# Performance work log

Measured on AMD Instinct MI355X. Metric: run time of the kernel, lower is better.

## Reference

```python
import jax, jax.numpy as jnp
import numpy as np

N = 8192
F_IN = 256
F_OUT = 64
ALPHA = 0.2  # LeakyReLU negative slope
NEG_INF = -9e15


def setup_inputs() -> dict:
    key = jax.random.key(0)
    k1, k2, k3, k4 = jax.random.split(key, 4)
    h = jax.random.normal(k1, (N, F_IN), dtype=jnp.float32)
    adj = jax.random.randint(k2, (N, N), 0, 2, dtype=jnp.int32)
    W = jax.random.normal(k3, (F_IN, F_OUT), dtype=jnp.float32) * 0.1
    a = jax.random.normal(k4, (2 * F_OUT, 1), dtype=jnp.float32) * 0.1
    return {"h": h, "adj": adj, "W": W, "a": a}


def reference(h, adj, W, a):
    # Wh: [N, F_out]
    Wh = h @ W
    # e_ij = LeakyReLU(a1 . Wh_i + a2 . Wh_j); same math as the O(N^2*2F)
    # concat in the original, computed via two [N] gathers + broadcast add.
    f_src = Wh @ a[:F_OUT, 0]   # [N] contribution of node i (row)
    f_dst = Wh @ a[F_OUT:, 0]   # [N] contribution of node j (col)
    e = f_src[:, None] + f_dst[None, :]          # [N, N]
    e = jnp.where(e > 0, e, ALPHA * e)           # LeakyReLU
    # masked softmax over neighbors (dim=1)
    e = jnp.where(adj > 0, e, NEG_INF)
    attention = jax.nn.softmax(e, axis=1)        # [N, N]
    h_prime = attention @ Wh                     # [N, F_out]
    # concat=True -> ELU
    return jax.nn.elu(h_prime)
```

## Files before the change

kernel.cpp:

```cpp
#include <hip/hip_runtime.h>
#include <math.h>

#define N 8192
#define FIN 256
#define FOUT 64
#define ALPHA 0.2f
#define LOG2E 1.442695040888963f

#define JT 256
#define NTILE (N / JT)
#define ROWPITCH 512
#define OFF_B 0
#define OFF_A (64 * ROWPITCH)
#define SMEM_BYTES (OFF_A + 16 * ROWPITCH)

typedef float f32x4 __attribute__((ext_vector_type(4)));
typedef _Float16 f16x8 __attribute__((ext_vector_type(8)));

__device__ __forceinline__ unsigned pack_f16(float a, float b) {
    union { _Float16 h; unsigned short u; } ca, cb;
    ca.h = (_Float16)a; cb.h = (_Float16)b;
    return (unsigned)ca.u | ((unsigned)cb.u << 16);
}
__device__ __forceinline__ float wcalc(int av, float fsr, float g) {
    float e = fsr + g;
    float le = e > 0.f ? e : ALPHA * e;
    float r = __builtin_exp2f(fmaf(le, LOG2E, -4.0f));
    return av != 0 ? r : 0.f;
}

__global__ __launch_bounds__(256) void gat_prep(
    const float* __restrict__ h, const float* __restrict__ W,
    const float* __restrict__ a,
    float* __restrict__ fsrc, float* __restrict__ fdst,
    unsigned short* __restrict__ WhT)
{
    __shared__ float sWh[16][FOUT + 1];
    const int t = threadIdx.x;
    const int f = t & 63;
    const int wq = t >> 6;
    const int row0 = blockIdx.x * 16;
    const int rbase = row0 + wq * 4;

    float acc[4] = {0.f, 0.f, 0.f, 0.f};
    for (int k0 = 0; k0 < FIN; k0 += 4) {
        const float w0 = W[(k0 + 0) * FOUT + f];
        const float w1 = W[(k0 + 1) * FOUT + f];
        const float w2 = W[(k0 + 2) * FOUT + f];
        const float w3 = W[(k0 + 3) * FOUT + f];
#pragma unroll
        for (int rr = 0; rr < 4; ++rr) {
            const float4 hv = *reinterpret_cast<const float4*>(
                &h[(size_t)(rbase + rr) * FIN + k0]);
            acc[rr] = fmaf(hv.x, w0, acc[rr]);
            acc[rr] = fmaf(hv.y, w1, acc[rr]);
            acc[rr] = fmaf(hv.z, w2, acc[rr]);
            acc[rr] = fmaf(hv.w, w3, acc[rr]);
        }
    }
    const float as = a[f], ad = a[FOUT + f];
#pragma unroll
    for (int rr = 0; rr < 4; ++rr) {
        sWh[wq * 4 + rr][f] = acc[rr];
        float fs = acc[rr] * as, fd = acc[rr] * ad;
#pragma unroll
        for (int off = 1; off < 64; off <<= 1) {
            fs += __shfl_xor(fs, off, 64);
            fd += __shfl_xor(fd, off, 64);
        }
        if (f == 0) { fsrc[rbase + rr] = fs; fdst[rbase + rr] = fd; }
    }
    __syncthreads();
    const int ff = t >> 2;
    const int r4 = (t & 3) * 4;
    uint2 v;
    v.x = pack_f16(sWh[r4 + 0][ff], sWh[r4 + 1][ff]);
    v.y = pack_f16(sWh[r4 + 2][ff], sWh[r4 + 3][ff]);
    *reinterpret_cast<uint2*>(&WhT[(size_t)ff * N + row0 + r4]) = v;
}

struct Regs { int4 a0, a1; float4 g0, g1; int4 b0, b1, b2, b3; };

__global__ __launch_bounds__(512, 4) void gat_main(
    const int* __restrict__ adj,
    const unsigned short* __restrict__ WhT,
    const float* __restrict__ fsrc, const float* __restrict__ fdst,
    float* __restrict__ out)
{
    __shared__ __align__(16) char smem[SMEM_BYTES];
    __shared__ float zbuf[16];

    const int t = threadIdx.x;
    const int l = t & 63;
    const int w = t >> 6;
    const int row0 = blockIdx.x * 16;

    const int srow = t >> 5;
    const int sc8 = (t & 31) * 8;
    const int bf = t >> 3;
    const int bg = t & 7;
    const float fsr = fsrc[row0 + srow];
    const size_t adjrow = (size_t)(row0 + srow) * N;
    const size_t bfrow = (size_t)bf * N;

    const int aswz = (srow & 7) << 4;
    const int bswz = (bf & 7) << 4;
    char* aw = smem + OFF_A + srow * ROWPITCH + (((t & 31) * 16) ^ aswz);
    char* bw0 = smem + OFF_B + bf * ROWPITCH + (((bg + 0) * 16) ^ bswz);
    char* bw1 = smem + OFF_B + bf * ROWPITCH + (((bg + 8) * 16) ^ bswz);
    char* bw2 = smem + OFF_B + bf * ROWPITCH + (((bg + 16) * 16) ^ bswz);
    char* bw3 = smem + OFF_B + bf * ROWPITCH + (((bg + 24) * 16) ^ bswz);

    const int ft = w & 3;
    const int p = w >> 2;
    const int r16 = l & 15;
    const int kg8 = (l >> 4) << 3;
    const int fswz = (r16 & 7) << 4;
    const char* ar = smem + OFF_A + r16 * ROWPITCH;
    const char* br = smem + OFF_B + (ft * 16 + r16) * ROWPITCH;

    f32x4 acc = {0.f, 0.f, 0.f, 0.f};
    float zacc = 0.f;
    Regs RA, RB;

#define LOADG(tile, S)                                                         \
    {                                                                          \
        const int j0_ = (tile) * JT;                                           \
        S.a0 = *reinterpret_cast<const int4*>(&adj[adjrow + j0_ + sc8]);       \
        S.a1 = *reinterpret_cast<const int4*>(&adj[adjrow + j0_ + sc8 + 4]);   \
        S.g0 = *reinterpret_cast<const float4*>(&fdst[j0_ + sc8]);             \
        S.g1 = *reinterpret_cast<const float4*>(&fdst[j0_ + sc8 + 4]);         \
        S.b0 = *reinterpret_cast<const int4*>(&WhT[bfrow + j0_ + (bg+0)*8]);   \
        S.b1 = *reinterpret_cast<const int4*>(&WhT[bfrow + j0_ + (bg+8)*8]);   \
        S.b2 = *reinterpret_cast<const int4*>(&WhT[bfrow + j0_ + (bg+16)*8]);  \
        S.b3 = *reinterpret_cast<const int4*>(&WhT[bfrow + j0_ + (bg+24)*8]);  \
    }

#define STAGE(S)                                                               \
    {                                                                          \
        *reinterpret_cast<int4*>(bw0) = S.b0;                                  \
        *reinterpret_cast<int4*>(bw1) = S.b1;                                  \
        *reinterpret_cast<int4*>(bw2) = S.b2;                                  \
        *reinterpret_cast<int4*>(bw3) = S.b3;                                  \
        const float w0 = wcalc(S.a0.x, fsr, S.g0.x);                           \
        const float w1 = wcalc(S.a0.y, fsr, S.g0.y);                           \
        const float w2 = wcalc(S.a0.z, fsr, S.g0.z);                           \
        const float w3 = wcalc(S.a0.w, fsr, S.g0.w);                           \
        const float w4 = wcalc(S.a1.x, fsr, S.g1.x);                           \
        const float w5 = wcalc(S.a1.y, fsr, S.g1.y);                           \
        const float w6 = wcalc(S.a1.z, fsr, S.g1.z);                           \
        const float w7 = wcalc(S.a1.w, fsr, S.g1.w);                           \
        zacc += (w0 + w1) + (w2 + w3) + ((w4 + w5) + (w6 + w7));               \
        uint4 pk;                                                              \
        pk.x = pack_f16(w0, w1); pk.y = pack_f16(w2, w3);                      \
        pk.z = pack_f16(w4, w5); pk.w = pack_f16(w6, w7);                      \
        *reinterpret_cast<uint4*>(aw) = pk;                                    \
    }

#define MFMA_PHASE                                                             \
    {                                                                          \
        __builtin_amdgcn_s_setprio(1);                                         \
        _Pragma("unroll")                                                      \
        for (int ks = 0; ks < 4; ++ks) {                                       \
            const int cb = (p * 128 + ks * 32 + kg8) * 2;                      \
            const f16x8 af = *reinterpret_cast<const f16x8*>(ar + (cb ^ fswz));\
            const f16x8 bfv = *reinterpret_cast<const f16x8*>(br + (cb ^ fswz));\
            acc = __builtin_amdgcn_mfma_f32_16x16x32_f16(af, bfv, acc, 0, 0, 0);\
        }                                                                      \
        __builtin_amdgcn_s_setprio(0);                                         \
    }

    LOADG(0, RA);
    LOADG(1, RB);
    for (int tt = 0; tt < NTILE; tt += 2) {
        STAGE(RA);
        if (tt + 2 < NTILE) LOADG(tt + 2, RA);
        __syncthreads();
        MFMA_PHASE;
        __syncthreads();
        STAGE(RB);
        if (tt + 3 < NTILE) LOADG(tt + 3, RB);
        __syncthreads();
        MFMA_PHASE;
        __syncthreads();
    }
#undef LOADG
#undef STAGE
#undef MFMA_PHASE

    {
        float z = zacc;
#pragma unroll
        for (int off = 1; off < 32; off <<= 1) z += __shfl_xor(z, off, 64);
        if ((l & 31) == 0) zbuf[srow] = z;
    }

    *reinterpret_cast<f32x4*>(smem + w * 1024 + l * 16) = acc;
    __syncthreads();
#pragma unroll
    for (int e0 = 0; e0 < 2; ++e0) {
        const int e = t + e0 * 512;
        const int rr = e >> 6, f2 = e & 63;
        const int ft2 = f2 >> 4, n = f2 & 15;
        const int ln = n | ((rr >> 2) << 4);
        const int rg = rr & 3;
        const float s =
            *reinterpret_cast<const float*>(smem + ft2 * 1024 + ln * 16 + rg * 4) +
            *reinterpret_cast<const float*>(smem + (ft2 + 4) * 1024 + ln * 16 + rg * 4);
        const float hp = s / zbuf[rr];
        out[(size_t)(row0 + rr) * FOUT + f2] = hp > 0.f ? hp : expm1f(hp);
    }
}

extern "C" void kernel_launch(void* const* d_in, const int* in_sizes, int n_in,
                              void* d_out, int out_size, void* d_ws, size_t ws_size,
                              hipStream_t stream) {
    const float* h   = (const float*)d_in[0];
    const int*   adj = (const int*)d_in[1];
    const float* W   = (const float*)d_in[2];
    const float* a   = (const float*)d_in[3];
    float* out = (float*)d_out;

    float* ws = (float*)d_ws;
    float* fsrc = ws;
    float* fdst = fsrc + N;
    unsigned short* WhT = (unsigned short*)(fdst + N);

    gat_prep<<<dim3(N / 16), dim3(256), 0, stream>>>(h, W, a, fsrc, fdst, WhT);
    gat_main<<<dim3(N / 16), dim3(512), 0, stream>>>(adj, WhT, fsrc, fdst, out);
}
```

Measured before the change: 97.20 us.

## Double-buffer LDS tiles and use one lightweight barrier per tile

```diff
diff --git a/kernel.cpp b/kernel.cpp
--- a/kernel.cpp
+++ b/kernel.cpp
@@ -12,7 +12,8 @@
 #define ROWPITCH 512
 #define OFF_B 0
 #define OFF_A (64 * ROWPITCH)
-#define SMEM_BYTES (OFF_A + 16 * ROWPITCH)
+#define BUFB (OFF_A + 16 * ROWPITCH)
+#define SMEM_BYTES (2 * BUFB)
 
 typedef float f32x4 __attribute__((ext_vector_type(4)));
 typedef _Float16 f16x8 __attribute__((ext_vector_type(8)));
@@ -88,7 +89,6 @@
     float* __restrict__ out)
 {
     __shared__ __align__(16) char smem[SMEM_BYTES];
-    __shared__ float zbuf[16];
 
     const int t = threadIdx.x;
     const int l = t & 63;
@@ -105,23 +105,29 @@
 
     const int aswz = (srow & 7) << 4;
     const int bswz = (bf & 7) << 4;
-    char* aw = smem + OFF_A + srow * ROWPITCH + (((t & 31) * 16) ^ aswz);
-    char* bw0 = smem + OFF_B + bf * ROWPITCH + (((bg + 0) * 16) ^ bswz);
-    char* bw1 = smem + OFF_B + bf * ROWPITCH + (((bg + 8) * 16) ^ bswz);
-    char* bw2 = smem + OFF_B + bf * ROWPITCH + (((bg + 16) * 16) ^ bswz);
-    char* bw3 = smem + OFF_B + bf * ROWPITCH + (((bg + 24) * 16) ^ bswz);
+    const int awo  = OFF_A + srow * ROWPITCH + (((t & 31) * 16) ^ aswz);
+    const int bwo0 = OFF_B + bf * ROWPITCH + (((bg + 0) * 16) ^ bswz);
+    const int bwo1 = OFF_B + bf * ROWPITCH + (((bg + 8) * 16) ^ bswz);
+    const int bwo2 = OFF_B + bf * ROWPITCH + (((bg + 16) * 16) ^ bswz);
+    const int bwo3 = OFF_B + bf * ROWPITCH + (((bg + 24) * 16) ^ bswz);
 
     const int ft = w & 3;
     const int p = w >> 2;
     const int r16 = l & 15;
     const int kg8 = (l >> 4) << 3;
     const int fswz = (r16 & 7) << 4;
-    const char* ar = smem + OFF_A + r16 * ROWPITCH;
-    const char* br = smem + OFF_B + (ft * 16 + r16) * ROWPITCH;
+    const int aro = OFF_A + r16 * ROWPITCH;
+    const int bro = OFF_B + (ft * 16 + r16) * ROWPITCH;
 
     f32x4 acc = {0.f, 0.f, 0.f, 0.f};
     float zacc = 0.f;
     Regs RA, RB;
+
+#define BAR                                                                    \
+    {                                                                          \
+        asm volatile("s_waitcnt lgkmcnt(0)" ::: "memory");                     \
+        __builtin_amdgcn_s_barrier();                                          \
+    }
 
 #define LOADG(tile, S)                                                         \
     {                                                                          \
@@ -136,12 +142,13 @@
         S.b3 = *reinterpret_cast<const int4*>(&WhT[bfrow + j0_ + (bg+24)*8]);  \
     }
 
-#define STAGE(S)                                                               \
-    {                                                                          \
-        *reinterpret_cast<int4*>(bw0) = S.b0;                                  \
-        *reinterpret_cast<int4*>(bw1) = S.b1;                                  \
-        *reinterpret_cast<int4*>(bw2) = S.b2;                                  \
-        *reinterpret_cast<int4*>(bw3) = S.b3;                                  \
+#define STAGE(S, BUF)                                                          \
+    {                                                                          \
+        char* bs_ = smem + (BUF) * BUFB;                                       \
+        *reinterpret_cast<int4*>(bs_ + bwo0) = S.b0;                           \
+        *reinterpret_cast<int4*>(bs_ + bwo1) = S.b1;                           \
+        *reinterpret_cast<int4*>(bs_ + bwo2) = S.b2;                           \
+        *reinterpret_cast<int4*>(bs_ + bwo3) = S.b3;                           \
         const float w0 = wcalc(S.a0.x, fsr, S.g0.x);                           \
         const float w1 = wcalc(S.a0.y, fsr, S.g0.y);                           \
         const float w2 = wcalc(S.a0.z, fsr, S.g0.z);                           \
@@ -154,45 +161,50 @@
         uint4 pk;                                                              \
         pk.x = pack_f16(w0, w1); pk.y = pack_f16(w2, w3);                      \
         pk.z = pack_f16(w4, w5); pk.w = pack_f16(w6, w7);                      \
-        *reinterpret_cast<uint4*>(aw) = pk;                                    \
-    }
-
-#define MFMA_PHASE                                                             \
-    {                                                                          \
+        *reinterpret_cast<uint4*>(bs_ + awo) = pk;                             \
+    }
+
+#define MFMA_PHASE(BUF)                                                        \
+    {                                                                          \
+        const char* bb_ = smem + (BUF) * BUFB;                                 \
         __builtin_amdgcn_s_setprio(1);                                         \
         _Pragma("unroll")                                                      \
         for (int ks = 0; ks < 4; ++ks) {                                       \
             const int cb = (p * 128 + ks * 32 + kg8) * 2;                      \
-            const f16x8 af = *reinterpret_cast<const f16x8*>(ar + (cb ^ fswz));\
-            const f16x8 bfv = *reinterpret_cast<const f16x8*>(br + (cb ^ fswz));\
-            acc = __builtin_amdgcn_mfma_f32_16x16x32_f16(af, bfv, acc, 0, 0, 0);\
+            const f16x8 af = *reinterpret_cast<const f16x8*>(bb_ + aro + (cb ^ fswz)); \
+            const f16x8 bv = *reinterpret_cast<const f16x8*>(bb_ + bro + (cb ^ fswz)); \
+            acc = __builtin_amdgcn_mfma_f32_16x16x32_f16(af, bv, acc, 0, 0, 0);\
         }                                                                      \
         __builtin_amdgcn_s_setprio(0);                                         \
     }
 
     LOADG(0, RA);
     LOADG(1, RB);
+    STAGE(RA, 0);
+    LOADG(2, RA);
+    BAR;
+
     for (int tt = 0; tt < NTILE; tt += 2) {
-        STAGE(RA);
-        if (tt + 2 < NTILE) LOADG(tt + 2, RA);
-        __syncthreads();
-        MFMA_PHASE;
-        __syncthreads();
-        STAGE(RB);
+        if (tt + 1 < NTILE) STAGE(RB, 1);
         if (tt + 3 < NTILE) LOADG(tt + 3, RB);
-        __syncthreads();
-        MFMA_PHASE;
-        __syncthreads();
+        MFMA_PHASE(0);
+        BAR;
+        if (tt + 2 < NTILE) STAGE(RA, 0);
+        if (tt + 4 < NTILE) LOADG(tt + 4, RA);
+        if (tt + 1 < NTILE) MFMA_PHASE(1);
+        BAR;
     }
 #undef LOADG
 #undef STAGE
 #undef MFMA_PHASE
-
+#undef BAR
+
+    float* zb = reinterpret_cast<float*>(smem + 8192);
     {
         float z = zacc;
 #pragma unroll
         for (int off = 1; off < 32; off <<= 1) z += __shfl_xor(z, off, 64);
-        if ((l & 31) == 0) zbuf[srow] = z;
+        if ((l & 31) == 0) zb[srow] = z;
     }
 
     *reinterpret_cast<f32x4*>(smem + w * 1024 + l * 16) = acc;
@@ -207,7 +219,7 @@
         const float s =
             *reinterpret_cast<const float*>(smem + ft2 * 1024 + ln * 16 + rg * 4) +
             *reinterpret_cast<const float*>(smem + (ft2 + 4) * 1024 + ln * 16 + rg * 4);
-        const float hp = s / zbuf[rr];
+        const float hp = s / zb[rr];
         out[(size_t)(row0 + rr) * FOUT + f2] = hp > 0.f ? hp : expm1f(hp);
     }
 }
```

After: 92.75 us. 4.6% less time.
